# Kernel optimization log

Measured on AMD Instinct MI355X. Metric: run time of the kernel, lower is better.

Reference implementation:

```python
import jax, jax.numpy as jnp
import numpy as np


def setup_inputs() -> dict:
    key = jax.random.key(0)
    x = jax.random.normal(key, (128, 256, 32, 32), dtype=jnp.float32)
    return {"x": x, "topk": 5}


def reference(x, topk):
    B = x.shape[0]
    flat = x.reshape(B, -1)                      # [B, N]
    _, idx = jax.lax.top_k(flat, topk)           # [B, k] indices into N
    out = jnp.zeros_like(flat)
    out = out.at[jnp.arange(B)[:, None], idx].set(1.0)
    return out.reshape(x.shape)
```

## Files before the change

kernel.cpp:

```cpp
#include <hip/hip_runtime.h>
#include <limits.h>
#include <math.h>
#include <stdint.h>

#define BROWS 128
#define NCOLS (256 * 32 * 32)
#define K 5
#define BPR 32
#define TPB 256
#define CHUNK (NCOLS / BPR)
#define C4 (CHUNK / 4)
#define F4T (C4 / TPB)
#define WPR (BPR * 4)
#define NFLAG 16
#define CAP 256

typedef float v4f __attribute__((ext_vector_type(4)));

__device__ __forceinline__ uint64_t make_key(float f, uint32_t idx) {
    uint32_t u = __float_as_uint(f);
    u = (u & 0x80000000u) ? ~u : (u | 0x80000000u);
    return ((uint64_t)u << 32) | (uint32_t)(~idx);
}
__device__ __forceinline__ uint32_t key_idx(uint64_t k) { return ~(uint32_t)k; }

#define KEY_NEG_INF 0x007FFFFF00000000ULL

__device__ __forceinline__ void insert5(uint64_t (&key)[K], uint64_t c) {
    if (c > key[K - 1]) {
        key[K - 1] = c;
#pragma unroll
        for (int s = K - 1; s > 0; --s) {
            if (key[s] > key[s - 1]) {
                uint64_t t = key[s]; key[s] = key[s - 1]; key[s - 1] = t;
            }
        }
    }
}

__device__ __forceinline__ void wave_reduce5(uint64_t (&key)[K]) {
#pragma unroll
    for (int off = 1; off < 64; off <<= 1) {
        uint64_t ok[K];
#pragma unroll
        for (int k = 0; k < K; ++k)
            ok[k] = __shfl_xor((unsigned long long)key[k], off, 64);
#pragma unroll
        for (int k = 0; k < K; ++k) insert5(key, ok[k]);
    }
}

__device__ __forceinline__ void insert5f(float (&v)[K], float c) {
    if (c > v[K - 1]) {
        v[K - 1] = c;
#pragma unroll
        for (int s = K - 1; s > 0; --s) {
            if (v[s] > v[s - 1]) { float t = v[s]; v[s] = v[s - 1]; v[s - 1] = t; }
        }
    }
}

__global__ __launch_bounds__(TPB) void wta_stream(const float* __restrict__ x,
                                                  float* __restrict__ out,
                                                  float* __restrict__ wmax) {
    const int gb = blockIdx.x;
    const size_t base = (size_t)gb * C4;
    const float4* __restrict__ x4 = (const float4*)x + base;
    float4* __restrict__ o4 = (float4*)out + base;
    const int t = threadIdx.x;
    const int lane = t & 63, w = t >> 6;
    const float4 z = {0.f, 0.f, 0.f, 0.f};

    float4 d[F4T];
#pragma unroll
    for (int j = 0; j < F4T; ++j) d[j] = x4[t + j * TPB];
#pragma unroll
    for (int j = 0; j < F4T; ++j) o4[t + j * TPB] = z;

    float M = -INFINITY;
#pragma unroll
    for (int j = 0; j < F4T; ++j)
        M = fmaxf(M, fmaxf(fmaxf(d[j].x, d[j].y), fmaxf(d[j].z, d[j].w)));
#pragma unroll
    for (int off = 1; off < 64; off <<= 1)
        M = fmaxf(M, __shfl_xor(M, off, 64));

    if (lane == 0) wmax[gb * 4 + w] = M;
}

__global__ __launch_bounds__(TPB) void wta_finish(const float* __restrict__ x,
                                                  const float* __restrict__ wmax,
                                                  float* __restrict__ out) {
    const int row = blockIdx.x;
    const int t = threadIdx.x;
    const float* __restrict__ wm = wmax + row * WPR;

    __shared__ float sT;
    __shared__ int nflag, ncand;
    __shared__ int flaglist[NFLAG];
    __shared__ uint64_t cand[CAP];

    if (t == 0) { nflag = 0; ncand = 0; }
    __syncthreads();

    if (t < 64) {
        float v[K];
#pragma unroll
        for (int k = 0; k < K; ++k) v[k] = -INFINITY;
        insert5f(v, wm[t]);
        insert5f(v, wm[t + 64]);
#pragma unroll
        for (int off = 1; off < 64; off <<= 1) {
            float ov[K];
#pragma unroll
            for (int k = 0; k < K; ++k) ov[k] = __shfl_xor(v[k], off, 64);
#pragma unroll
            for (int k = 0; k < K; ++k) insert5f(v, ov[k]);
        }
        if (t == 0) sT = v[K - 1];
    }
    __syncthreads();
    const float T = sT;

    if (t < WPR && wm[t] >= T) {
        const int s = atomicAdd(&nflag, 1);
        if (s < NFLAG) flaglist[s] = t;
    }
    __syncthreads();
    const int nf = min(nflag, NFLAG);

    const int lane = t & 63, jj = t >> 6;
    for (int f = 0; f < nf; ++f) {
        const int wid = flaglist[f];
        const int gbk = wid >> 2;
        const int w   = wid & 3;
        const float4* __restrict__ xb =
            (const float4*)(x + (size_t)row * NCOLS + (size_t)gbk * CHUNK);
#pragma unroll
        for (int rep = 0; rep < 2; ++rep) {
            const int j = jj + rep * 4;
            const int f4pos = w * 64 + lane + j * TPB;
            const float4 d = xb[f4pos];
            const float vs[4] = {d.x, d.y, d.z, d.w};
#pragma unroll
            for (int c = 0; c < 4; ++c) {
                if (vs[c] >= T) {
                    const int s = atomicAdd(&ncand, 1);
                    if (s < CAP)
                        cand[s] = make_key(vs[c],
                                           (uint32_t)gbk * CHUNK + (uint32_t)f4pos * 4u + c);
                }
            }
        }
    }
    __syncthreads();

    if (t < 64) {
        const int n = min(ncand, CAP);
        uint64_t key[K];
#pragma unroll
        for (int k = 0; k < K; ++k) key[k] = KEY_NEG_INF;
        for (int i = t; i < n; i += 64) insert5(key, cand[i]);
        wave_reduce5(key);
        if (t == 0) {
#pragma unroll
            for (int k = 0; k < K; ++k)
                if (key[k] != KEY_NEG_INF)
                    out[(size_t)row * NCOLS + key_idx(key[k])] = 1.0f;
        }
    }
}

extern "C" void kernel_launch(void* const* d_in, const int* in_sizes, int n_in,
                              void* d_out, int out_size, void* d_ws, size_t ws_size,
                              hipStream_t stream) {
    const float* x = (const float*)d_in[0];
    float* out = (float*)d_out;

    float* wmax = (float*)d_ws;

    wta_stream<<<BROWS * BPR, TPB, 0, stream>>>(x, out, wmax);
    wta_finish<<<BROWS, TPB, 0, stream>>>(x, wmax, out);
}
```

Baseline: 243.6 us.

## Use contiguous 256-element span maxima with grid-stride scan and memset output zeroing

Replaces the per-block strided stream kernel with a grid-stride scan where each wave computes the max of a contiguous 256-float span, giving 1024 span maxima per row. The zero fill of the output moves from in-kernel stores to hipMemsetAsync. The finish kernel selects the threshold from the 1024 maxima and rescans only the flagged spans, one wave per span, so the rescan work is much smaller. This trades a larger threshold-selection step and an extra memset launch for finer-grained candidate spans and a lighter scan kernel.

Result: no change. 239.9 us (-1.5%).

```diff
diff --git a/kernel.cpp b/kernel.cpp
--- a/kernel.cpp
+++ b/kernel.cpp
@@ -6,16 +6,14 @@
 #define BROWS 128
 #define NCOLS (256 * 32 * 32)
 #define K 5
-#define BPR 32
 #define TPB 256
-#define CHUNK (NCOLS / BPR)
-#define C4 (CHUNK / 4)
-#define F4T (C4 / TPB)
-#define WPR (BPR * 4)
-#define NFLAG 16
+#define SPANS_PER_ROW 1024
+#define SPAN 256
+#define SCAN_BLOCKS 2048
+#define SCAN_ITERS 16
+#define STRIDE4 (SCAN_BLOCKS * TPB)
+#define NFLAG 32
 #define CAP 256
-
-typedef float v4f __attribute__((ext_vector_type(4)));
 
 __device__ __forceinline__ uint64_t make_key(float f, uint32_t idx) {
     uint32_t u = __float_as_uint(f);
@@ -60,32 +58,29 @@
     }
 }
 
-__global__ __launch_bounds__(TPB) void wta_stream(const float* __restrict__ x,
-                                                  float* __restrict__ out,
-                                                  float* __restrict__ wmax) {
-    const int gb = blockIdx.x;
-    const size_t base = (size_t)gb * C4;
-    const float4* __restrict__ x4 = (const float4*)x + base;
-    float4* __restrict__ o4 = (float4*)out + base;
+__global__ __launch_bounds__(TPB) void wta_scan(const float* __restrict__ x,
+                                                float* __restrict__ wmax) {
     const int t = threadIdx.x;
+    const int g = blockIdx.x * TPB + t;
     const int lane = t & 63, w = t >> 6;
-    const float4 z = {0.f, 0.f, 0.f, 0.f};
+    const int waveid = blockIdx.x * 4 + w;
+    const float4* __restrict__ x4 = (const float4*)x;
 
-    float4 d[F4T];
+    float m[SCAN_ITERS];
 #pragma unroll
-    for (int j = 0; j < F4T; ++j) d[j] = x4[t + j * TPB];
+    for (int i = 0; i < SCAN_ITERS; ++i) {
+        const float4 v = x4[(size_t)g + (size_t)i * STRIDE4];
+        m[i] = fmaxf(fmaxf(v.x, v.y), fmaxf(v.z, v.w));
+    }
+
 #pragma unroll
-    for (int j = 0; j < F4T; ++j) o4[t + j * TPB] = z;
-
-    float M = -INFINITY;
+    for (int i = 0; i < SCAN_ITERS; ++i) {
+        float M = m[i];
 #pragma unroll
-    for (int j = 0; j < F4T; ++j)
-        M = fmaxf(M, fmaxf(fmaxf(d[j].x, d[j].y), fmaxf(d[j].z, d[j].w)));
-#pragma unroll
-    for (int off = 1; off < 64; off <<= 1)
-        M = fmaxf(M, __shfl_xor(M, off, 64));
-
-    if (lane == 0) wmax[gb * 4 + w] = M;
+        for (int off = 1; off < 64; off <<= 1)
+            M = fmaxf(M, __shfl_xor(M, off, 64));
+        if (lane == 0) wmax[waveid + i * (SCAN_BLOCKS * 4)] = M;
+    }
 }
 
 __global__ __launch_bounds__(TPB) void wta_finish(const float* __restrict__ x,
@@ -93,7 +88,7 @@
                                                   float* __restrict__ out) {
     const int row = blockIdx.x;
     const int t = threadIdx.x;
-    const float* __restrict__ wm = wmax + row * WPR;
+    const float* __restrict__ wm = wmax + (size_t)row * SPANS_PER_ROW;
 
     __shared__ float sT;
     __shared__ int nflag, ncand;
@@ -107,8 +102,8 @@
         float v[K];
 #pragma unroll
         for (int k = 0; k < K; ++k) v[k] = -INFINITY;
-        insert5f(v, wm[t]);
-        insert5f(v, wm[t + 64]);
+#pragma unroll
+        for (int i = 0; i < SPANS_PER_ROW / 64; ++i) insert5f(v, wm[t + i * 64]);
 #pragma unroll
         for (int off = 1; off < 64; off <<= 1) {
             float ov[K];
@@ -122,34 +117,28 @@
     __syncthreads();
     const float T = sT;
 
-    if (t < WPR && wm[t] >= T) {
-        const int s = atomicAdd(&nflag, 1);
-        if (s < NFLAG) flaglist[s] = t;
+    for (int s = t; s < SPANS_PER_ROW; s += TPB) {
+        if (wm[s] >= T) {
+            const int p = atomicAdd(&nflag, 1);
+            if (p < NFLAG) flaglist[p] = s;
+        }
     }
     __syncthreads();
     const int nf = min(nflag, NFLAG);
 
-    const int lane = t & 63, jj = t >> 6;
-    for (int f = 0; f < nf; ++f) {
-        const int wid = flaglist[f];
-        const int gbk = wid >> 2;
-        const int w   = wid & 3;
-        const float4* __restrict__ xb =
-            (const float4*)(x + (size_t)row * NCOLS + (size_t)gbk * CHUNK);
+    const int lane = t & 63, w4 = t >> 6;
+    for (int f = w4; f < nf; f += 4) {
+        const int sp = flaglist[f];
+        const float4 d =
+            ((const float4*)(x + (size_t)row * NCOLS + (size_t)sp * SPAN))[lane];
+        const float vs[4] = {d.x, d.y, d.z, d.w};
 #pragma unroll
-        for (int rep = 0; rep < 2; ++rep) {
-            const int j = jj + rep * 4;
-            const int f4pos = w * 64 + lane + j * TPB;
-            const float4 d = xb[f4pos];
-            const float vs[4] = {d.x, d.y, d.z, d.w};
-#pragma unroll
-            for (int c = 0; c < 4; ++c) {
-                if (vs[c] >= T) {
-                    const int s = atomicAdd(&ncand, 1);
-                    if (s < CAP)
-                        cand[s] = make_key(vs[c],
-                                           (uint32_t)gbk * CHUNK + (uint32_t)f4pos * 4u + c);
-                }
+        for (int c = 0; c < 4; ++c) {
+            if (vs[c] >= T) {
+                const int p = atomicAdd(&ncand, 1);
+                if (p < CAP)
+                    cand[p] = make_key(vs[c],
+                                       (uint32_t)sp * SPAN + (uint32_t)lane * 4u + c);
             }
         }
     }
@@ -179,6 +168,8 @@
 
     float* wmax = (float*)d_ws;
 
-    wta_stream<<<BROWS * BPR, TPB, 0, stream>>>(x, out, wmax);
+    hipMemsetAsync(d_out, 0, (size_t)out_size, stream);
+
+    wta_scan<<<SCAN_BLOCKS, TPB, 0, stream>>>(x, wmax);
     wta_finish<<<BROWS, TPB, 0, stream>>>(x, wmax, out);
 }
```
